# Optimization experiments

Hardware: AMD Instinct MI355X
Metric: run time of the kernel (lower is better)

Reference implementation:

```python
import jax, jax.numpy as jnp
import numpy as np
import math

D_MODEL = 1024
N_HEAD = 16
D_HEAD = D_MODEL // N_HEAD
D_KMAP = 128
D_INNER = 4096


def setup_inputs() -> dict:
    key = jax.random.key(0)
    ks = jax.random.split(key, 12)
    s = 0.02
    return {
        "x": jax.random.normal(ks[0], (4, 4096, D_MODEL), dtype=jnp.float32),
        "proj_mat": jax.random.normal(ks[1], (D_HEAD, D_KMAP), dtype=jnp.float32),
        "wq": jax.random.normal(ks[2], (D_MODEL, D_MODEL), dtype=jnp.float32) * s,
        "bq": jnp.zeros((D_MODEL,), jnp.float32),
        "wk": jax.random.normal(ks[3], (D_MODEL, D_MODEL), dtype=jnp.float32) * s,
        "bk": jnp.zeros((D_MODEL,), jnp.float32),
        "wv": jax.random.normal(ks[4], (D_MODEL, D_MODEL), dtype=jnp.float32) * s,
        "bv": jnp.zeros((D_MODEL,), jnp.float32),
        "wo": jax.random.normal(ks[5], (D_MODEL, D_MODEL), dtype=jnp.float32) * s,
        "bo": jnp.zeros((D_MODEL,), jnp.float32),
        "ln1_g": jnp.ones((D_MODEL,), jnp.float32),
        "ln1_b": jnp.zeros((D_MODEL,), jnp.float32),
        "w1": jax.random.normal(ks[6], (D_MODEL, D_INNER), dtype=jnp.float32) * s,
        "b1": jnp.zeros((D_INNER,), jnp.float32),
        "w2": jax.random.normal(ks[7], (D_INNER, D_MODEL), dtype=jnp.float32) * s,
        "b2": jnp.zeros((D_MODEL,), jnp.float32),
        "ln2_g": jnp.ones((D_MODEL,), jnp.float32),
        "ln2_b": jnp.zeros((D_MODEL,), jnp.float32),
    }


def _layer_norm(x, g, b, eps=1e-5):
    mu = jnp.mean(x, axis=-1, keepdims=True)
    var = jnp.mean(jnp.square(x - mu), axis=-1, keepdims=True)
    return (x - mu) * jax.lax.rsqrt(var + eps) * g + b


def _fourier_kernel(x, proj_mat):
    # x: [B, L, H, d_head] -> [B, L, H, 2*d_kmap]
    p = jnp.einsum('blhd,dm->blhm', x, proj_mat) / math.sqrt(D_HEAD)
    return jnp.concatenate([jnp.cos(p), jnp.sin(p)], axis=-1) / math.sqrt(D_KMAP)


def reference(x, proj_mat, wq, bq, wk, bk, wv, bv, wo, bo,
              ln1_g, ln1_b, w1, b1, w2, b2, ln2_g, ln2_b):
    B, L, _ = x.shape
    # pre-norm linear attention
    x2 = _layer_norm(x, ln1_g, ln1_b)
    q = (x2 @ wq + bq).reshape(B, L, N_HEAD, D_HEAD)
    k = (x2 @ wk + bk).reshape(B, L, N_HEAD, D_HEAD)
    v = (x2 @ wv + bv).reshape(B, L, N_HEAD, D_HEAD)
    qp = _fourier_kernel(q, proj_mat)  # [B,L,H,2M]
    kp = _fourier_kernel(k, proj_mat)
    kv = jnp.einsum('blhm,blhd->bhmd', kp, v)      # [B,H,2M,Dh]
    attn = jnp.einsum('blhm,bhmd->blhd', qp, kv)   # [B,L,H,Dh]
    attn = attn.reshape(B, L, D_MODEL) @ wo + bo
    x = x + attn  # dropout is identity in eval
    # FFN
    x2 = _layer_norm(x, ln2_g, ln2_b)
    h = jax.nn.relu(x2 @ w1 + b1)
    x = x + (h @ w2 + b2)
    return x
```

## Files before the change

### kernel.cpp

```cpp
#include <hip/hip_runtime.h>


#define RS128 0.08838834764831845f

typedef short bf16x8 __attribute__((ext_vector_type(8)));
typedef float f32x4 __attribute__((ext_vector_type(4)));

__device__ __forceinline__ unsigned short f2bf(float f) {
  unsigned int u = __float_as_uint(f);
  u += 0x7fffu + ((u >> 16) & 1u);
  return (unsigned short)(u >> 16);
}
__device__ __forceinline__ float bf2f(unsigned short h) {
  return __uint_as_float(((unsigned int)h) << 16);
}
__device__ __forceinline__ unsigned int pack2f(float a, float b) {
  return (unsigned int)f2bf(a) | ((unsigned int)f2bf(b) << 16);
}
__device__ __forceinline__ void gload_lds16(const void* g, void* l) {
  __builtin_amdgcn_global_load_lds(
      (const __attribute__((address_space(1))) void*)g,
      (__attribute__((address_space(3))) void*)l, 16, 0, 0);
}
__device__ __forceinline__ void barrier_pin() {
  __builtin_amdgcn_sched_barrier(0);
  __builtin_amdgcn_s_barrier();
  __builtin_amdgcn_sched_barrier(0);
}
#define WAIT_VM(N) { asm volatile("s_waitcnt vmcnt(" #N ")" ::: "memory"); __builtin_amdgcn_sched_barrier(0); }
#define WAIT_LGKM0() { asm volatile("s_waitcnt lgkmcnt(0)" ::: "memory"); __builtin_amdgcn_sched_barrier(0); }

template <bool OBF16, bool RELU, bool RES, bool PROJ, bool TRANSV>
__global__ __launch_bounds__(512, 2) void gemm256(
    const unsigned short* __restrict__ A, const unsigned short* __restrict__ Bt,
    void* Cv, const float* __restrict__ bias, const float* res,
    const unsigned short* __restrict__ projTs, int M, int N, int K) {
  __shared__ __align__(16) char lds[163840];
  const int tid = threadIdx.x;
  const int lane = tid & 63, wid = tid >> 6;
  const int e = lane & 15, g = lane >> 4;
  const int wm = wid >> 1, wn = wid & 1;
  const int ntn = N >> 7;
  const int nwg = (int)gridDim.x, cpx = nwg >> 3;
  const int swz = ((int)blockIdx.x & 7) * cpx + ((int)blockIdx.x >> 3);
  const int bm = swz / ntn, bn = swz % ntn;
  const long row0 = (long)bm << 8, col0 = (long)bn << 7;

  const int srow = tid >> 3;
  const int skb = ((tid & 7) << 4) ^ ((srow & 7) << 4);
  const unsigned short* Abase = A + (row0 + srow) * (long)K + (skb >> 1);
  const unsigned short* Bbase = Bt + (col0 + srow) * (long)K + (skb >> 1);
  const int lof = wid << 10;

  f32x4 acc[4][4] = {};
  const int nkt = K >> 6;
  const int rx = (e & 7) << 4;

  char* bufA = lds;
  char* bufB = lds + 49152;
  char* bufC = lds + 98304;

  if (PROJ) {
    gload_lds16((const char*)projTs + (wid << 10) + (lane << 4),
                lds + 147456 + (wid << 10));
    gload_lds16((const char*)projTs + 8192 + (wid << 10) + (lane << 4),
                lds + 147456 + 8192 + (wid << 10));
  }
#pragma unroll
  for (int c = 0; c < 4; ++c)
    gload_lds16(Abase + (long)c * 64 * K, bufA + lof + c * 8192);
#pragma unroll
  for (int c = 0; c < 2; ++c)
    gload_lds16(Bbase + (long)c * 64 * K, bufA + 32768 + lof + c * 8192);
#pragma unroll
  for (int c = 0; c < 4; ++c)
    gload_lds16(Abase + (long)c * 64 * K + 64, bufB + lof + c * 8192);
#pragma unroll
  for (int c = 0; c < 2; ++c)
    gload_lds16(Bbase + (long)c * 64 * K + 64, bufB + 32768 + lof + c * 8192);
  WAIT_VM(6);
  barrier_pin();

  for (int kt = 0; kt < nkt; ++kt) {
    char* Ac = bufA;
    char* Bc = bufA + 32768;
    const bool pf2 = (kt + 2 < nkt);
    const long kn2 = (long)(kt + 2) << 6;

    bf16x8 bfr[4][2];
#pragma unroll
    for (int j = 0; j < 4; ++j) {
      const int r = wn * 64 + j * 16 + e;
#pragma unroll
      for (int kh = 0; kh < 2; ++kh)
        bfr[j][kh] = *(const bf16x8*)(Bc + r * 128 + ((g * 16 + kh * 64) ^ rx));
    }
    bf16x8 af0[2][2];
#pragma unroll
    for (int i = 0; i < 2; ++i) {
      const int r = wm * 64 + i * 16 + e;
#pragma unroll
      for (int kh = 0; kh < 2; ++kh)
        af0[i][kh] = *(const bf16x8*)(Ac + r * 128 + ((g * 16 + kh * 64) ^ rx));
    }
    if (pf2) {
#pragma unroll
      for (int c = 0; c < 3; ++c)
        gload_lds16(Abase + (long)c * 64 * K + kn2, bufC + lof + c * 8192);
    }
    barrier_pin();
    WAIT_LGKM0();
    __builtin_amdgcn_s_setprio(1);
#pragma unroll
    for (int i = 0; i < 2; ++i)
#pragma unroll
      for (int j = 0; j < 4; ++j)
#pragma unroll
        for (int kh = 0; kh < 2; ++kh)
          acc[i][j] = __builtin_amdgcn_mfma_f32_16x16x32_bf16(
              af0[i][kh], bfr[j][kh], acc[i][j], 0, 0, 0);
    __builtin_amdgcn_s_setprio(0);
    barrier_pin();

    bf16x8 af1[2][2];
#pragma unroll
    for (int i = 0; i < 2; ++i) {
      const int r = wm * 64 + (2 + i) * 16 + e;
#pragma unroll
      for (int kh = 0; kh < 2; ++kh)
        af1[i][kh] = *(const bf16x8*)(Ac + r * 128 + ((g * 16 + kh * 64) ^ rx));
    }
    if (pf2) {
      gload_lds16(Abase + (long)3 * 64 * K + kn2, bufC + lof + 3 * 8192);
      gload_lds16(Bbase + kn2, bufC + 32768 + lof);
      gload_lds16(Bbase + (long)64 * K + kn2, bufC + 32768 + lof + 8192);
      WAIT_VM(6);
    } else if (kt + 1 < nkt) {
      WAIT_VM(0);
    }
    barrier_pin();
    WAIT_LGKM0();
    __builtin_amdgcn_s_setprio(1);
#pragma unroll
    for (int i = 0; i < 2; ++i)
#pragma unroll
      for (int j = 0; j < 4; ++j)
#pragma unroll
        for (int kh = 0; kh < 2; ++kh)
          acc[2 + i][j] = __builtin_amdgcn_mfma_f32_16x16x32_bf16(
              af1[i][kh], bfr[j][kh], acc[2 + i][j], 0, 0, 0);
    __builtin_amdgcn_s_setprio(0);
    barrier_pin();

    char* t = bufA; bufA = bufB; bufB = bufC; bufC = t;
  }

  if (PROJ) {
    char* qt = lds + (wid << 13);
    const int c0p = wn * 64 + e;
#pragma unroll
    for (int j = 0; j < 4; ++j) {
      const float bvv = bias[col0 + c0p + (j << 4)];
#pragma unroll
      for (int mf = 0; mf < 4; ++mf)
#pragma unroll
        for (int r = 0; r < 4; ++r) {
          const int lrow = (mf << 4) + (g << 2) + r;
          const int dby = ((((j << 4) + e) << 1)) ^ ((lrow & 7) << 4);
          *(unsigned short*)(qt + lrow * 128 + dby) = f2bf(acc[mf][j][r] + bvv);
        }
    }
    WAIT_LGKM0();
    const char* pj = lds + 147456;
    bf16x8 paf[4][2];
#pragma unroll
    for (int i = 0; i < 4; ++i) {
      const int r = (i << 4) + e;
#pragma unroll
      for (int kh = 0; kh < 2; ++kh)
        paf[i][kh] = *(const bf16x8*)(qt + r * 128 + ((g * 16 + kh * 64) ^ rx));
    }
    f32x4 pacc[4][8] = {};
#pragma unroll
    for (int j = 0; j < 8; ++j) {
      const int m = (j << 4) + e;
      const bf16x8 pb0 = *(const bf16x8*)(pj + m * 128 + ((g * 16) ^ rx));
      const bf16x8 pb1 = *(const bf16x8*)(pj + m * 128 + ((g * 16 + 64) ^ rx));
#pragma unroll
      for (int i = 0; i < 4; ++i) {
        pacc[i][j] = __builtin_amdgcn_mfma_f32_16x16x32_bf16(paf[i][0], pb0,
                                                             pacc[i][j], 0, 0, 0);
        pacc[i][j] = __builtin_amdgcn_mfma_f32_16x16x32_bf16(paf[i][1], pb1,
                                                             pacc[i][j], 0, 0, 0);
      }
    }
    unsigned short* PHp = (unsigned short*)Cv;
    const int hh = 2 * bn + wn;
    const long lbase = row0 + wm * 64;
#pragma unroll
    for (int i = 0; i < 4; ++i)
#pragma unroll
      for (int j = 0; j < 8; ++j)
#pragma unroll
        for (int r = 0; r < 4; ++r) {
          const long l = lbase + (i << 4) + (g << 2) + r;
          PHp[l * 2048 + hh * 128 + (j << 4) + e] = f2bf(pacc[i][j][r]);
        }
    return;
  }

  if (TRANSV) {
    unsigned short* qt = (unsigned short*)(lds + (wid << 13));
#pragma unroll
    for (int j = 0; j < 4; ++j) {
      const int dcol = (j << 4) + e;
      const float bvv = bias[col0 + wn * 64 + dcol];
#pragma unroll
      for (int mf = 0; mf < 4; ++mf)
#pragma unroll
        for (int r = 0; r < 4; ++r) {
          const int lr = (mf << 4) + (g << 2) + r;
          qt[lr * 64 + (dcol ^ ((lr & 7) << 1))] = f2bf(acc[mf][j][r] + bvv);
        }
    }
    WAIT_LGKM0();
    const int b = (int)(row0 >> 12);
    const int hh = 2 * bn + wn;
    const int lb0 = ((int)(row0 & 4095)) + wm * 64;
    const int d = lane;
    char* basep = (char*)Cv + (((long)(b * 16 + hh) * 64 + d) * 4096 + lb0) * 2;
#pragma unroll
    for (int cc8 = 0; cc8 < 8; ++cc8) {
      unsigned short v[8];
#pragma unroll
      for (int k = 0; k < 8; ++k)
        v[k] = qt[(cc8 * 8 + k) * 64 + (d ^ (k << 1))];
      uint4 o;
      o.x = (unsigned)v[0] | ((unsigned)v[1] << 16);
      o.y = (unsigned)v[2] | ((unsigned)v[3] << 16);
      o.z = (unsigned)v[4] | ((unsigned)v[5] << 16);
      o.w = (unsigned)v[6] | ((unsigned)v[7] << 16);
      *(uint4*)(basep + ((cc8 ^ (d & 7)) << 4)) = o;
    }
    return;
  }

  const int r0 = wm * 64 + (g << 2);
  const int c0 = wn * 64 + e;
#pragma unroll
  for (int j = 0; j < 4; ++j) {
    const long gcol = col0 + c0 + (j << 4);
    const float bvv = bias[gcol];
#pragma unroll
    for (int mf = 0; mf < 4; ++mf) {
#pragma unroll
      for (int r = 0; r < 4; ++r) {
        const long grow = row0 + r0 + (mf << 4) + r;
        float v = acc[mf][j][r] + bvv;
        if (RES) v += res[grow * N + gcol];
        if (RELU) v = fmaxf(v, 0.f);
        if (OBF16) ((unsigned short*)Cv)[grow * N + gcol] = f2bf(v);
        else ((float*)Cv)[grow * N + gcol] = v;
      }
    }
  }
}

__global__ __launch_bounds__(256) void wtrans(const float* __restrict__ W,
                                              unsigned short* __restrict__ Wt,
                                              int K, int N) {
  __shared__ float t[32][33];
  const int tx = threadIdx.x & 31, ty = threadIdx.x >> 5;
  const int n0 = blockIdx.x << 5, k0 = blockIdx.y << 5;
#pragma unroll
  for (int i = 0; i < 32; i += 8)
    t[ty + i][tx] = W[(long)(k0 + ty + i) * N + n0 + tx];
  __syncthreads();
#pragma unroll
  for (int i = 0; i < 32; i += 8)
    Wt[(long)(n0 + ty + i) * K + k0 + tx] = f2bf(t[tx][ty + i]);
}

__global__ __launch_bounds__(256) void projt_prep(const float* __restrict__ proj,
                                                  unsigned short* __restrict__ projTs) {
  const int t = threadIdx.x;
  const int m = t >> 1, sh = t & 1;
#pragma unroll
  for (int s4 = 0; s4 < 4; ++s4) {
    const int s = sh * 4 + s4;
    unsigned short v[8];
#pragma unroll
    for (int k = 0; k < 8; ++k)
      v[k] = f2bf(proj[(s * 8 + k) * 128 + m] * 0.125f);
    uint4 o;
    o.x = (unsigned)v[0] | ((unsigned)v[1] << 16);
    o.y = (unsigned)v[2] | ((unsigned)v[3] << 16);
    o.z = (unsigned)v[4] | ((unsigned)v[5] << 16);
    o.w = (unsigned)v[6] | ((unsigned)v[7] << 16);
    *(uint4*)((char*)projTs + m * 128 + ((s ^ (m & 7)) << 4)) = o;
  }
}

__global__ __launch_bounds__(256) void ln_kernel(const float* __restrict__ x,
                                                 const float* __restrict__ g,
                                                 const float* __restrict__ b,
                                                 unsigned short* __restrict__ out) {
  const int row = blockIdx.x, tid = threadIdx.x;
  const float* xr = x + (long)row * 1024;
  const float4 xv = *(const float4*)(xr + tid * 4);
  float s = xv.x + xv.y + xv.z + xv.w;
  float s2 = xv.x * xv.x + xv.y * xv.y + xv.z * xv.z + xv.w * xv.w;
#pragma unroll
  for (int off = 32; off > 0; off >>= 1) {
    s += __shfl_down(s, off);
    s2 += __shfl_down(s2, off);
  }
  __shared__ float ps[4], ps2[4];
  if ((tid & 63) == 0) { ps[tid >> 6] = s; ps2[tid >> 6] = s2; }
  __syncthreads();
  const float ts = ps[0] + ps[1] + ps[2] + ps[3];
  const float ts2 = ps2[0] + ps2[1] + ps2[2] + ps2[3];
  const float mu = ts * (1.f / 1024.f);
  const float rstd = rsqrtf(ts2 * (1.f / 1024.f) - mu * mu + 1e-5f);
  const float4 gv = *(const float4*)(g + tid * 4);
  const float4 bv = *(const float4*)(b + tid * 4);
  ushort4 o;
  o.x = f2bf((xv.x - mu) * rstd * gv.x + bv.x);
  o.y = f2bf((xv.y - mu) * rstd * gv.y + bv.y);
  o.z = f2bf((xv.z - mu) * rstd * gv.z + bv.z);
  o.w = f2bf((xv.w - mu) * rstd * gv.w + bv.w);
  *(ushort4*)(out + (long)row * 1024 + tid * 4) = o;
}

__global__ __launch_bounds__(256, 2) void kv_kernel(
    const unsigned short* __restrict__ PH, const unsigned short* __restrict__ VTg,
    float* __restrict__ PART, int half) {
  __shared__ __align__(16) unsigned short Ps[64 * 128];
  __shared__ __align__(16) unsigned short Vs[64 * 64];
  __shared__ __align__(16) unsigned short KPT[256 * 64];
  const int tid = threadIdx.x;
  const int lane = tid & 63, wid = tid >> 6;
  const int bhh = blockIdx.x, chunk = blockIdx.y;
  const int b2 = bhh >> 4, h = bhh & 15;
  const int bh = (half * 2 + b2) * 16 + h;

  f32x4 acc[4][4] = {};
  const int e = lane & 15, g = lane >> 4;
  const int m = tid & 127, isin = tid >> 7;
  const int m2 = (isin << 7) + m, swm = m & 7;

  for (int ti = 0; ti < 4; ++ti) {
    const int l0 = chunk * 256 + ti * 64;
    __syncthreads();
#pragma unroll
    for (int c = 0; c < 4; ++c) {
      const int r = l0 + c * 16 + (tid >> 4);
      gload_lds16((const char*)PH + (long)(b2 * 4096 + r) * 4096 + h * 256 + (tid & 15) * 16,
                  (char*)Ps + c * 4096 + (wid << 10));
    }
#pragma unroll
    for (int c = 0; c < 2; ++c) {
      const int d = c * 32 + (tid >> 3);
      gload_lds16((const char*)VTg + ((long)(bh * 64 + d) * 4096 + l0) * 2 + (tid & 7) * 16,
                  (char*)Vs + c * 4096 + (wid << 10));
    }
    __syncthreads();
    {
      char* krow = (char*)KPT + m2 * 128;
#pragma unroll
      for (int g8 = 0; g8 < 8; ++g8) {
        unsigned pk[4];
#pragma unroll
        for (int k2 = 0; k2 < 4; ++k2) {
          const float p0 = bf2f(Ps[(g8 * 8 + k2 * 2) * 128 + m]);
          const float p1 = bf2f(Ps[(g8 * 8 + k2 * 2 + 1) * 128 + m]);
          const float v0 = (isin ? __sinf(p0) : __cosf(p0)) * RS128;
          const float v1 = (isin ? __sinf(p1) : __cosf(p1)) * RS128;
          pk[k2] = pack2f(v0, v1);
        }
        uint4 o; o.x = pk[0]; o.y = pk[1]; o.z = pk[2]; o.w = pk[3];
        *(uint4*)(krow + ((g8 ^ swm) << 4)) = o;
      }
    }
    __syncthreads();
#pragma unroll
    for (int kk = 0; kk < 2; ++kk) {
      const int ch = (kk << 2) + g;
      bf16x8 af[4], bfr[4];
#pragma unroll
      for (int i = 0; i < 4; ++i) {
        const int dr = (i << 4) + e;
        af[i] = *(const bf16x8*)((char*)Vs + dr * 128 + ((ch ^ (e & 7)) << 4));
      }
#pragma unroll
      for (int j = 0; j < 4; ++j) {
        const int mr = (wid << 6) + (j << 4) + e;
        bfr[j] = *(const bf16x8*)((char*)KPT + mr * 128 + ((ch ^ (e & 7)) << 4));
      }
#pragma unroll
      for (int i = 0; i < 4; ++i)
#pragma unroll
        for (int j = 0; j < 4; ++j)
          acc[i][j] = __builtin_amdgcn_mfma_f32_16x16x32_bf16(af[i], bfr[j],
                                                              acc[i][j], 0, 0, 0);
    }
  }
  float* slice = PART + ((long)chunk * 32 + bhh) * 16384;
#pragma unroll
  for (int i = 0; i < 4; ++i)
#pragma unroll
    for (int j = 0; j < 4; ++j)
#pragma unroll
      for (int r = 0; r < 4; ++r) {
        const int d = (i << 4) + (g << 2) + r;
        const int mc = (wid << 6) + (j << 4) + e;
        slice[d * 256 + mc] = acc[i][j][r];
      }
}

__global__ __launch_bounds__(256) void kv_reduce(const float* __restrict__ PART,
                                                 float* __restrict__ KVacc, int half) {
  const int bhh = blockIdx.x, seg = blockIdx.y;
  const long off = (long)bhh * 16384 + seg * 1024 + threadIdx.x * 4;
  float4 s = make_float4(0.f, 0.f, 0.f, 0.f);
#pragma unroll
  for (int c = 0; c < 16; ++c) {
    const float4 v = *(const float4*)(PART + ((long)c * 32) * 16384 + off);
    s.x += v.x; s.y += v.y; s.z += v.z; s.w += v.w;
  }
  *(float4*)(KVacc + (long)(half * 32) * 16384 + off) = s;
}

__global__ __launch_bounds__(256) void kvt_conv(const float* __restrict__ KVacc,
                                                unsigned short* __restrict__ KVT) {
  const int bh = blockIdx.x, tid = threadIdx.x;
  const int d = tid >> 2, mq = tid & 3;
  const float* src = KVacc + (long)bh * 16384 + d * 256 + mq * 64;
  char* dst = (char*)KVT + bh * 32768 + d * 512;
#pragma unroll
  for (int cc = 0; cc < 8; ++cc) {
    const float4 a = *(const float4*)(src + cc * 8);
    const float4 b = *(const float4*)(src + cc * 8 + 4);
    uint4 o;
    o.x = pack2f(a.x, a.y); o.y = pack2f(a.z, a.w);
    o.z = pack2f(b.x, b.y); o.w = pack2f(b.z, b.w);
    const int chunk = mq * 8 + cc;
    *(uint4*)(dst + ((chunk ^ (d & 7)) << 4)) = o;
  }
}

__global__ __launch_bounds__(256, 2) void attn_kernel(
    const unsigned short* __restrict__ PH, const unsigned short* __restrict__ KVT,
    unsigned short* __restrict__ ATTN, int half) {
  __shared__ __align__(16) unsigned short QPs[64 * 256];
  __shared__ __align__(16) unsigned short KVs[64 * 256];
  const int tid = threadIdx.x;
  const int lane = tid & 63, wid = tid >> 6;
  const int bhh = blockIdx.x, chunk = blockIdx.y;
  const int b2 = bhh >> 4, h = bhh & 15;
  const int b = half * 2 + b2, bh = b * 16 + h;
  const int e = lane & 15, g = lane >> 4;

#pragma unroll
  for (int c = 0; c < 8; ++c)
    gload_lds16((const char*)KVT + bh * 32768 + c * 4096 + tid * 16,
                (char*)KVs + c * 4096 + (wid << 10));

  const int lrow = tid >> 2, ms = tid & 3, swl = lrow & 7;

  for (int ti = 0; ti < 4; ++ti) {
    const int l0 = chunk * 256 + ti * 64;
    const char* pg = (const char*)PH + (long)(b2 * 4096 + l0 + lrow) * 4096 + h * 256 + ms * 64;
    uint4 P[4];
#pragma unroll
    for (int q = 0; q < 4; ++q) P[q] = *(const uint4*)(pg + q * 16);
    uint4 CQ[4], SQ[4];
#pragma unroll
    for (int q = 0; q < 4; ++q) {
      const unsigned w[4] = {P[q].x, P[q].y, P[q].z, P[q].w};
      unsigned cw[4], sw[4];
#pragma unroll
      for (int k = 0; k < 4; ++k) {
        float c0, s0, c1, s1;
        __sincosf(bf2f((unsigned short)(w[k] & 0xffff)), &s0, &c0);
        __sincosf(bf2f((unsigned short)(w[k] >> 16)), &s1, &c1);
        cw[k] = pack2f(c0 * RS128, c1 * RS128);
        sw[k] = pack2f(s0 * RS128, s1 * RS128);
      }
      CQ[q].x = cw[0]; CQ[q].y = cw[1]; CQ[q].z = cw[2]; CQ[q].w = cw[3];
      SQ[q].x = sw[0]; SQ[q].y = sw[1]; SQ[q].z = sw[2]; SQ[q].w = sw[3];
    }
    __syncthreads();
    {
      char* qrow = (char*)QPs + lrow * 512;
#pragma unroll
      for (int q = 0; q < 4; ++q) {
        const int c = ms * 4 + q;
        *(uint4*)(qrow + ((c ^ swl) << 4)) = CQ[q];
        *(uint4*)(qrow + ((16 + (c ^ swl)) << 4)) = SQ[q];
      }
    }
    __syncthreads();
    f32x4 acc[4] = {};
    const int lr = (wid << 4) + e;
#pragma unroll
    for (int kk = 0; kk < 8; ++kk) {
      const int ch = (kk << 2) + g;
      const bf16x8 af = *(const bf16x8*)((char*)QPs + lr * 512 + ((ch ^ (e & 7)) << 4));
#pragma unroll
      for (int j = 0; j < 4; ++j) {
        const bf16x8 bfr = *(const bf16x8*)((char*)KVs + ((j << 4) + e) * 512 + ((ch ^ (e & 7)) << 4));
        acc[j] = __builtin_amdgcn_mfma_f32_16x16x32_bf16(af, bfr, acc[j], 0, 0, 0);
      }
    }
#pragma unroll
    for (int j = 0; j < 4; ++j)
#pragma unroll
      for (int r = 0; r < 4; ++r) {
        const int lo = (wid << 4) + (g << 2) + r;
        ATTN[(long)(b * 4096 + l0 + lo) * 1024 + h * 64 + (j << 4) + e] = f2bf(acc[j][r]);
      }
  }
}

extern "C" void kernel_launch(void* const* d_in, const int* in_sizes, int n_in,
                              void* d_out, int out_size, void* d_ws, size_t ws_size,
                              hipStream_t stream) {
  (void)in_sizes; (void)n_in; (void)out_size; (void)ws_size;
  const float* x    = (const float*)d_in[0];
  const float* proj = (const float*)d_in[1];
  const float* wq = (const float*)d_in[2];
  const float* bq = (const float*)d_in[3];
  const float* wk = (const float*)d_in[4];
  const float* bk = (const float*)d_in[5];
  const float* wv = (const float*)d_in[6];
  const float* bv = (const float*)d_in[7];
  const float* wo = (const float*)d_in[8];
  const float* bo = (const float*)d_in[9];
  const float* g1  = (const float*)d_in[10];
  const float* be1 = (const float*)d_in[11];
  const float* w1 = (const float*)d_in[12];
  const float* b1 = (const float*)d_in[13];
  const float* w2 = (const float*)d_in[14];
  const float* b2 = (const float*)d_in[15];
  const float* g2  = (const float*)d_in[16];
  const float* be2 = (const float*)d_in[17];
  float* out = (float*)d_out;

  char* ws = (char*)d_ws;
  const size_t MB = 1u << 20;
  unsigned short* WQT    = (unsigned short*)(ws + 0 * MB);
  unsigned short* WKT    = (unsigned short*)(ws + 2 * MB);
  unsigned short* WVT    = (unsigned short*)(ws + 4 * MB);
  unsigned short* WOT    = (unsigned short*)(ws + 6 * MB);
  unsigned short* projTs = (unsigned short*)(ws + 8 * MB);
  float* KVacc = (float*)(ws + 10 * MB);
  unsigned short* KVT = (unsigned short*)(ws + 14 * MB);
  unsigned short* VTg  = (unsigned short*)(ws + 16 * MB);
  unsigned short* PH   = (unsigned short*)(ws + 64 * MB);
  float* PART  = (float*)(ws + 96 * MB);
  unsigned short* Hb  = (unsigned short*)(ws + 0 * MB);
  unsigned short* X2  = (unsigned short*)(ws + 128 * MB);
  unsigned short* W1T = (unsigned short*)(ws + 160 * MB);
  unsigned short* W2T = (unsigned short*)(ws + 168 * MB);
  unsigned short* ATTN = VTg;
  unsigned short* X2B  = X2;

  dim3 blk(256), blk5(512);

  wtrans<<<dim3(32, 32), blk, 0, stream>>>(wq, WQT, 1024, 1024);
  wtrans<<<dim3(32, 32), blk, 0, stream>>>(wk, WKT, 1024, 1024);
  wtrans<<<dim3(32, 32), blk, 0, stream>>>(wv, WVT, 1024, 1024);
  wtrans<<<dim3(32, 32), blk, 0, stream>>>(wo, WOT, 1024, 1024);
  wtrans<<<dim3(128, 32), blk, 0, stream>>>(w1, W1T, 1024, 4096);
  wtrans<<<dim3(32, 128), blk, 0, stream>>>(w2, W2T, 4096, 1024);
  projt_prep<<<1, blk, 0, stream>>>(proj, projTs);

  ln_kernel<<<16384, blk, 0, stream>>>(x, g1, be1, X2);

  gemm256<false, false, false, false, true><<<512, blk5, 0, stream>>>(
      X2, WVT, VTg, bv, nullptr, nullptr, 16384, 1024, 1024);

  for (int half = 0; half < 2; ++half) {
    gemm256<true, false, false, true, false><<<256, blk5, 0, stream>>>(
        X2 + (long)half * 8192 * 1024, WKT, PH, bk, nullptr, projTs, 8192, 1024, 1024);
    kv_kernel<<<dim3(32, 16), blk, 0, stream>>>(PH, VTg, PART, half);
    kv_reduce<<<dim3(32, 16), blk, 0, stream>>>(PART, KVacc, half);
  }
  kvt_conv<<<64, blk, 0, stream>>>(KVacc, KVT);

  for (int half = 0; half < 2; ++half) {
    gemm256<true, false, false, true, false><<<256, blk5, 0, stream>>>(
        X2 + (long)half * 8192 * 1024, WQT, PH, bq, nullptr, projTs, 8192, 1024, 1024);
    attn_kernel<<<dim3(32, 16), blk, 0, stream>>>(PH, KVT, ATTN, half);
  }

  gemm256<false, false, true, false, false><<<512, blk5, 0, stream>>>(
      ATTN, WOT, out, bo, x, nullptr, 16384, 1024, 1024);

  ln_kernel<<<16384, blk, 0, stream>>>(out, g2, be2, X2B);

  gemm256<true, true, false, false, false><<<2048, blk5, 0, stream>>>(
      X2B, W1T, Hb, b1, nullptr, nullptr, 16384, 4096, 1024);
  gemm256<false, false, true, false, false><<<512, blk5, 0, stream>>>(
      Hb, W2T, out, b2, out, nullptr, 16384, 1024, 4096);
}
```

Before: 732.4 us.

## Run FFN GEMMs in FP8 with scaled MFMA and FP8 LayerNorm output

After: 614.0 us. -16.2%, faster.

```diff
diff --git a/kernel.cpp b/kernel.cpp
--- a/kernel.cpp
+++ b/kernel.cpp
@@ -5,6 +5,8 @@
 
 typedef short bf16x8 __attribute__((ext_vector_type(8)));
 typedef float f32x4 __attribute__((ext_vector_type(4)));
+typedef int i32x4v __attribute__((ext_vector_type(4)));
+typedef int i32x8v __attribute__((ext_vector_type(8)));
 
 __device__ __forceinline__ unsigned short f2bf(float f) {
   unsigned int u = __float_as_uint(f);
@@ -29,6 +31,18 @@
 }
 #define WAIT_VM(N) { asm volatile("s_waitcnt vmcnt(" #N ")" ::: "memory"); __builtin_amdgcn_sched_barrier(0); }
 #define WAIT_LGKM0() { asm volatile("s_waitcnt lgkmcnt(0)" ::: "memory"); __builtin_amdgcn_sched_barrier(0); }
+
+__device__ __forceinline__ i32x8v mk8(i32x4v lo, i32x4v hi) {
+  i32x8v v;
+  v[0] = lo[0]; v[1] = lo[1]; v[2] = lo[2]; v[3] = lo[3];
+  v[4] = hi[0]; v[5] = hi[1]; v[6] = hi[2]; v[7] = hi[3];
+  return v;
+}
+__device__ __forceinline__ unsigned int pk4fp8(float a, float b, float c, float d) {
+  int p = __builtin_amdgcn_cvt_pk_fp8_f32(a, b, 0, false);
+  p = __builtin_amdgcn_cvt_pk_fp8_f32(c, d, p, true);
+  return (unsigned int)p;
+}
 
 template <bool OBF16, bool RELU, bool RES, bool PROJ, bool TRANSV>
 __global__ __launch_bounds__(512, 2) void gemm256(
@@ -266,6 +280,156 @@
   }
 }
 
+template <bool OFP8, int SB>
+__global__ __launch_bounds__(512, 2) void gemm256f8(
+    const char* __restrict__ A, const char* __restrict__ Bt,
+    void* Cv, const float* __restrict__ bias, const float* res,
+    int M, int N, int K) {
+  __shared__ __align__(16) char lds[147456];
+  const int tid = threadIdx.x;
+  const int lane = tid & 63, wid = tid >> 6;
+  const int e = lane & 15, g = lane >> 4;
+  const int wm = wid >> 1, wn = wid & 1;
+  const int ntn = N >> 7;
+  const int nwg = (int)gridDim.x, cpx = nwg >> 3;
+  const int swz = ((int)blockIdx.x & 7) * cpx + ((int)blockIdx.x >> 3);
+  const int bm = swz / ntn, bn = swz % ntn;
+  const long row0 = (long)bm << 8, col0 = (long)bn << 7;
+
+  const int srow = tid >> 3;
+  const int skb = ((tid & 7) << 4) ^ ((srow & 7) << 4);
+  const char* Abase = A + (row0 + srow) * (long)K + skb;
+  const char* Bbase = Bt + (col0 + srow) * (long)K + skb;
+  const int lof = wid << 10;
+
+  f32x4 acc[4][4] = {};
+  const int nkt = K >> 7;
+  const int rx = (e & 7) << 4;
+
+  char* bufA = lds;
+  char* bufB = lds + 49152;
+  char* bufC = lds + 98304;
+
+#pragma unroll
+  for (int c = 0; c < 4; ++c)
+    gload_lds16(Abase + (long)c * 64 * K, bufA + lof + c * 8192);
+#pragma unroll
+  for (int c = 0; c < 2; ++c)
+    gload_lds16(Bbase + (long)c * 64 * K, bufA + 32768 + lof + c * 8192);
+#pragma unroll
+  for (int c = 0; c < 4; ++c)
+    gload_lds16(Abase + (long)c * 64 * K + 128, bufB + lof + c * 8192);
+#pragma unroll
+  for (int c = 0; c < 2; ++c)
+    gload_lds16(Bbase + (long)c * 64 * K + 128, bufB + 32768 + lof + c * 8192);
+  WAIT_VM(6);
+  barrier_pin();
+
+  for (int kt = 0; kt < nkt; ++kt) {
+    char* Ac = bufA;
+    char* Bc = bufA + 32768;
+    const bool pf2 = (kt + 2 < nkt);
+    const long kn2 = (long)(kt + 2) << 7;
+
+    i32x8v bfr[4];
+#pragma unroll
+    for (int j = 0; j < 4; ++j) {
+      const int r = wn * 64 + j * 16 + e;
+      const i32x4v lo = *(const i32x4v*)(Bc + r * 128 + ((g * 32) ^ rx));
+      const i32x4v hi = *(const i32x4v*)(Bc + r * 128 + ((g * 32 + 16) ^ rx));
+      bfr[j] = mk8(lo, hi);
+    }
+    i32x8v af0[2];
+#pragma unroll
+    for (int i = 0; i < 2; ++i) {
+      const int r = wm * 64 + i * 16 + e;
+      const i32x4v lo = *(const i32x4v*)(Ac + r * 128 + ((g * 32) ^ rx));
+      const i32x4v hi = *(const i32x4v*)(Ac + r * 128 + ((g * 32 + 16) ^ rx));
+      af0[i] = mk8(lo, hi);
+    }
+    if (pf2) {
+#pragma unroll
+      for (int c = 0; c < 3; ++c)
+        gload_lds16(Abase + (long)c * 64 * K + kn2, bufC + lof + c * 8192);
+    }
+    barrier_pin();
+    WAIT_LGKM0();
+    __builtin_amdgcn_s_setprio(1);
+#pragma unroll
+    for (int i = 0; i < 2; ++i)
+#pragma unroll
+      for (int j = 0; j < 4; ++j)
+        acc[i][j] = __builtin_amdgcn_mfma_scale_f32_16x16x128_f8f6f4(
+            af0[i], bfr[j], acc[i][j], 0, 0, 0, 127, 0, SB);
+    __builtin_amdgcn_s_setprio(0);
+    barrier_pin();
+
+    i32x8v af1[2];
+#pragma unroll
+    for (int i = 0; i < 2; ++i) {
+      const int r = wm * 64 + (2 + i) * 16 + e;
+      const i32x4v lo = *(const i32x4v*)(Ac + r * 128 + ((g * 32) ^ rx));
+      const i32x4v hi = *(const i32x4v*)(Ac + r * 128 + ((g * 32 + 16) ^ rx));
+      af1[i] = mk8(lo, hi);
+    }
+    if (pf2) {
+      gload_lds16(Abase + (long)3 * 64 * K + kn2, bufC + lof + 3 * 8192);
+      gload_lds16(Bbase + kn2, bufC + 32768 + lof);
+      gload_lds16(Bbase + (long)64 * K + kn2, bufC + 32768 + lof + 8192);
+      WAIT_VM(6);
+    } else if (kt + 1 < nkt) {
+      WAIT_VM(0);
+    }
+    barrier_pin();
+    WAIT_LGKM0();
+    __builtin_amdgcn_s_setprio(1);
+#pragma unroll
+    for (int i = 0; i < 2; ++i)
+#pragma unroll
+      for (int j = 0; j < 4; ++j)
+        acc[2 + i][j] = __builtin_amdgcn_mfma_scale_f32_16x16x128_f8f6f4(
+            af1[i], bfr[j], acc[2 + i][j], 0, 0, 0, 127, 0, SB);
+    __builtin_amdgcn_s_setprio(0);
+    barrier_pin();
+
+    char* t = bufA; bufA = bufB; bufB = bufC; bufC = t;
+  }
+
+  const int r0 = wm * 64 + (g << 2);
+  const int c0 = wn * 64 + e;
+  if (OFP8) {
+    unsigned char* O = (unsigned char*)Cv;
+#pragma unroll
+    for (int j = 0; j < 4; ++j) {
+      const long gcol = col0 + c0 + (j << 4);
+      const float bvv = bias[gcol];
+#pragma unroll
+      for (int mf = 0; mf < 4; ++mf)
+#pragma unroll
+        for (int r = 0; r < 4; ++r) {
+          const long grow = row0 + r0 + (mf << 4) + r;
+          const float v = fmaxf(acc[mf][j][r] + bvv, 0.f);
+          O[grow * (long)N + gcol] =
+              (unsigned char)(__builtin_amdgcn_cvt_pk_fp8_f32(v, v, 0, false) & 0xFF);
+        }
+    }
+  } else {
+    float* O = (float*)Cv;
+#pragma unroll
+    for (int j = 0; j < 4; ++j) {
+      const long gcol = col0 + c0 + (j << 4);
+      const float bvv = bias[gcol];
+#pragma unroll
+      for (int mf = 0; mf < 4; ++mf)
+#pragma unroll
+        for (int r = 0; r < 4; ++r) {
+          const long grow = row0 + r0 + (mf << 4) + r;
+          O[grow * (long)N + gcol] = acc[mf][j][r] + bvv + res[grow * (long)N + gcol];
+        }
+    }
+  }
+}
+
 __global__ __launch_bounds__(256) void wtrans(const float* __restrict__ W,
                                               unsigned short* __restrict__ Wt,
                                               int K, int N) {
@@ -279,6 +443,22 @@
 #pragma unroll
   for (int i = 0; i < 32; i += 8)
     Wt[(long)(n0 + ty + i) * K + k0 + tx] = f2bf(t[tx][ty + i]);
+}
+
+__global__ __launch_bounds__(256) void wtrans8(const float* __restrict__ W,
+                                               unsigned char* __restrict__ Wt,
+                                               int K, int N, float scale) {
+  __shared__ float t[32][33];
+  const int tx = threadIdx.x & 31, ty = threadIdx.x >> 5;
+  const int n0 = blockIdx.x << 5, k0 = blockIdx.y << 5;
+#pragma unroll
+  for (int i = 0; i < 32; i += 8)
+    t[ty + i][tx] = W[(long)(k0 + ty + i) * N + n0 + tx];
+  __syncthreads();
+  const int n = threadIdx.x >> 3, kq = threadIdx.x & 7;
+  const unsigned int p = pk4fp8(t[kq * 4 + 0][n] * scale, t[kq * 4 + 1][n] * scale,
+                                t[kq * 4 + 2][n] * scale, t[kq * 4 + 3][n] * scale);
+  *(unsigned int*)(Wt + (long)(n0 + n) * K + k0 + kq * 4) = p;
 }
 
 __global__ __launch_bounds__(256) void projt_prep(const float* __restrict__ proj,
@@ -330,6 +510,36 @@
   o.z = f2bf((xv.z - mu) * rstd * gv.z + bv.z);
   o.w = f2bf((xv.w - mu) * rstd * gv.w + bv.w);
   *(ushort4*)(out + (long)row * 1024 + tid * 4) = o;
+}
+
+__global__ __launch_bounds__(256) void ln_kernel8(const float* __restrict__ x,
+                                                  const float* __restrict__ g,
+                                                  const float* __restrict__ b,
+                                                  unsigned char* __restrict__ out) {
+  const int row = blockIdx.x, tid = threadIdx.x;
+  const float* xr = x + (long)row * 1024;
+  const float4 xv = *(const float4*)(xr + tid * 4);
+  float s = xv.x + xv.y + xv.z + xv.w;
+  float s2 = xv.x * xv.x + xv.y * xv.y + xv.z * xv.z + xv.w * xv.w;
+#pragma unroll
+  for (int off = 32; off > 0; off >>= 1) {
+    s += __shfl_down(s, off);
+    s2 += __shfl_down(s2, off);
+  }
+  __shared__ float ps[4], ps2[4];
+  if ((tid & 63) == 0) { ps[tid >> 6] = s; ps2[tid >> 6] = s2; }
+  __syncthreads();
+  const float ts = ps[0] + ps[1] + ps[2] + ps[3];
+  const float ts2 = ps2[0] + ps2[1] + ps2[2] + ps2[3];
+  const float mu = ts * (1.f / 1024.f);
+  const float rstd = rsqrtf(ts2 * (1.f / 1024.f) - mu * mu + 1e-5f);
+  const float4 gv = *(const float4*)(g + tid * 4);
+  const float4 bv = *(const float4*)(b + tid * 4);
+  const unsigned int p = pk4fp8((xv.x - mu) * rstd * gv.x + bv.x,
+                                (xv.y - mu) * rstd * gv.y + bv.y,
+                                (xv.z - mu) * rstd * gv.z + bv.z,
+                                (xv.w - mu) * rstd * gv.w + bv.w);
+  *(unsigned int*)(out + (long)row * 1024 + tid * 4) = p;
 }
 
 __global__ __launch_bounds__(256, 2) void kv_kernel(
@@ -559,12 +769,12 @@
   unsigned short* VTg  = (unsigned short*)(ws + 16 * MB);
   unsigned short* PH   = (unsigned short*)(ws + 64 * MB);
   float* PART  = (float*)(ws + 96 * MB);
-  unsigned short* Hb  = (unsigned short*)(ws + 0 * MB);
-  unsigned short* X2  = (unsigned short*)(ws + 128 * MB);
-  unsigned short* W1T = (unsigned short*)(ws + 160 * MB);
-  unsigned short* W2T = (unsigned short*)(ws + 168 * MB);
+  unsigned char* Hb8   = (unsigned char*)(ws + 0 * MB);
+  unsigned short* X2   = (unsigned short*)(ws + 128 * MB);
+  unsigned char* X2B8  = (unsigned char*)(ws + 128 * MB);
+  unsigned char* W1T8  = (unsigned char*)(ws + 160 * MB);
+  unsigned char* W2T8  = (unsigned char*)(ws + 164 * MB);
   unsigned short* ATTN = VTg;
-  unsigned short* X2B  = X2;
 
   dim3 blk(256), blk5(512);
 
@@ -572,8 +782,8 @@
   wtrans<<<dim3(32, 32), blk, 0, stream>>>(wk, WKT, 1024, 1024);
   wtrans<<<dim3(32, 32), blk, 0, stream>>>(wv, WVT, 1024, 1024);
   wtrans<<<dim3(32, 32), blk, 0, stream>>>(wo, WOT, 1024, 1024);
-  wtrans<<<dim3(128, 32), blk, 0, stream>>>(w1, W1T, 1024, 4096);
-  wtrans<<<dim3(32, 128), blk, 0, stream>>>(w2, W2T, 4096, 1024);
+  wtrans8<<<dim3(128, 32), blk, 0, stream>>>(w1, W1T8, 1024, 4096, 16.f);
+  wtrans8<<<dim3(32, 128), blk, 0, stream>>>(w2, W2T8, 4096, 1024, 16.f);
   projt_prep<<<1, blk, 0, stream>>>(proj, projTs);
 
   ln_kernel<<<16384, blk, 0, stream>>>(x, g1, be1, X2);
@@ -598,10 +808,10 @@
   gemm256<false, false, true, false, false><<<512, blk5, 0, stream>>>(
       ATTN, WOT, out, bo, x, nullptr, 16384, 1024, 1024);
 
-  ln_kernel<<<16384, blk, 0, stream>>>(out, g2, be2, X2B);
-
-  gemm256<true, true, false, false, false><<<2048, blk5, 0, stream>>>(
-      X2B, W1T, Hb, b1, nullptr, nullptr, 16384, 4096, 1024);
-  gemm256<false, false, true, false, false><<<512, blk5, 0, stream>>>(
-      Hb, W2T, out, b2, out, nullptr, 16384, 1024, 4096);
-}
+  ln_kernel8<<<16384, blk, 0, stream>>>(out, g2, be2, X2B8);
+
+  gemm256f8<true, 123><<<2048, blk5, 0, stream>>>(
+      (const char*)X2B8, (const char*)W1T8, Hb8, b1, nullptr, 16384, 4096, 1024);
+  gemm256f8<false, 123><<<512, blk5, 0, stream>>>(
+      (const char*)Hb8, (const char*)W2T8, out, b2, out, 16384, 1024, 4096);
+}
```
